# Optimization experiments

Hardware: AMD Instinct MI355X
Metric: run time of the kernel (lower is better)

## Reference

```python
import jax, jax.numpy as jnp
import numpy as np

ATT_RANGE = 10
R_FACTOR = 2
NHEAD = 8

def softsign(x):
    return x / (1.0 + jnp.abs(x))

def layer_norm(x, g, b, eps=1e-5):
    mu = jnp.mean(x, axis=-1, keepdims=True)
    var = jnp.var(x, axis=-1, keepdims=True)
    return (x - mu) / jnp.sqrt(var + eps) * g + b

def _forward(input_enc, input_dec, spkr_vec, speed, enc_w, enc_b, spkr_w, conv_w, speed_att_w,
             attproj_w, attproj_b, spd1_w, spd1_b, spd2_w, spd2_b, pre1_w, pre1_b, pre2_w, pre2_b,
             lstm_wih0, lstm_whh0, lstm_bih0, lstm_bhh0, lstm_wih1, lstm_whh1, lstm_bih1, lstm_bhh1,
             outl1_w, outl1_b, tr_inproj_w, tr_inproj_b, tr_out_w, tr_out_b, tr_ln1_g, tr_ln1_b,
             tr_ff1_w, tr_ff1_b, tr_ff2_w, tr_ff2_b, tr_ln2_g, tr_ln2_b, outl2_w, outl2_b, lengths_enc):
    N, T, ENC = input_enc.shape
    # first-step attention state: one-hot at t=0 (null_state branch)
    aw0 = jnp.zeros((N, T), input_enc.dtype).at[:, 0].set(1.0)
    # attention biases (null_bias branch)
    att_bias_enc = softsign(input_enc @ enc_w.T + enc_b)          # (N,T,ATT)
    att_bias_spkr = softsign(spkr_vec @ spkr_w.T)                  # (N,1,ATT)
    in_att_speed = (speed[:, None] @ speed_att_w.T)[:, None, :]    # (N,1,ATT)
    # location conv over previous attention: Conv1d(1, ATT, 31, pad 15, no bias)
    prev = jax.lax.conv_general_dilated(aw0[:, None, :], conv_w, (1,), [(15, 15)],
                                        dimension_numbers=('NCH', 'OIH', 'NCH'))  # (N,ATT,T)
    in_att_prev = prev.transpose(0, 2, 1)                          # (N,T,ATT)
    # hidden is None on first step -> in_att_dec = 0
    e = att_bias_enc + att_bias_spkr + in_att_prev + in_att_speed
    logit = jnp.tanh(e) @ attproj_w.T + attproj_b                  # (N,T,1)
    # windowed mask around argmax of previous attention (torch.no_grad)
    m = jnp.argmax(aw0, axis=1)                                    # (N,)
    t = jnp.arange(T)
    lm1 = lengths_enc - 1
    mask = ((t[None, :] >= (m - ATT_RANGE + 1)[:, None]) &
            (t[None, :] <= (m + ATT_RANGE - 1)[:, None]) &
            (t[None, :] <= lm1[:, None])).astype(logit.dtype)[..., None]
    w = jnp.exp(logit - jnp.max(logit, axis=1, keepdims=True)) * jax.lax.stop_gradient(mask)
    w = w / jnp.maximum(jnp.sum(jnp.abs(w), axis=1, keepdims=True), 1e-12)  # F.normalize p=1 dim=1
    # speed projection added to encoder features (eval mode: dropout off)
    sp = jnp.tanh(jax.nn.relu(speed[:, None] @ spd1_w.T + spd1_b) @ spd2_w.T + spd2_b)  # (N,ENC)
    enc2 = input_enc + sp[:, None, :]
    context = jnp.einsum('nt,ntc->nc', w[..., 0], enc2)[:, None, :]  # (N,1,ENC)
    # prenet on cat(input_dec, spkr)
    pin = jnp.concatenate([input_dec, spkr_vec[:, 0, :]], axis=-1)
    pre = jax.nn.relu(jax.nn.relu(pin @ pre1_w.T + pre1_b) @ pre2_w.T + pre2_b)[:, None, :]
    in_lstm = jnp.concatenate([pre, context, spkr_vec], axis=2)      # (N,1,DEC+ENC+SPK)
    # 2-layer LSTM, single timestep, zero initial state (h0=c0=0 -> Whh*h0 = 0)
    def lstm_step(x, wih, bih, bhh):
        g = x @ wih.T + bih + bhh
        i, f, gg, o = jnp.split(g, 4, axis=-1)
        c = jax.nn.sigmoid(i) * jnp.tanh(gg)
        return jax.nn.sigmoid(o) * jnp.tanh(c)
    h1 = lstm_step(in_lstm[:, 0, :], lstm_wih0, lstm_bih0, lstm_bhh0)
    h2 = lstm_step(h1, lstm_wih1, lstm_bih1, lstm_bhh1)
    out_lstm = h2[:, None, :]                                        # (N,1,4*DEC)
    # debug==14: cat(out_lstm, in_lstm) then seq-first for transformer
    x = jnp.concatenate([out_lstm, in_lstm], axis=2).transpose(1, 0, 2)  # (1,N,3136)
    x = x @ outl1_w.T + outl1_b                                      # (1,N,DEC)
    D = x.shape[-1]
    dh = D // NHEAD
    for l in range(tr_inproj_w.shape[0]):
        qkv = x @ tr_inproj_w[l].T + tr_inproj_b[l]
        q, k, v = jnp.split(qkv, 3, axis=-1)
        S, Nn, _ = q.shape
        qh = q.reshape(S, Nn, NHEAD, dh)
        kh = k.reshape(S, Nn, NHEAD, dh)
        vh = v.reshape(S, Nn, NHEAD, dh)
        a = jnp.einsum('snhd,tnhd->nhst', qh, kh) / jnp.sqrt(jnp.asarray(dh, x.dtype))
        a = jax.nn.softmax(a, axis=-1)
        att = jnp.einsum('nhst,tnhd->snhd', a, vh).reshape(S, Nn, D)
        att = att @ tr_out_w[l].T + tr_out_b[l]
        x = layer_norm(x + att, tr_ln1_g[l], tr_ln1_b[l])
        ff = jax.nn.relu(x @ tr_ff1_w[l].T + tr_ff1_b[l]) @ tr_ff2_w[l].T + tr_ff2_b[l]
        x = layer_norm(x + ff, tr_ln2_g[l], tr_ln2_b[l])
    out = (x @ outl2_w.T + outl2_b).transpose(1, 0, 2).reshape(N, R_FACTOR, -1)  # (N,2,80)
    return out, context

def setup_inputs():
    key = jax.random.key(0)
    ks = iter(jax.random.split(key, 64))
    def nrm(shape, s=0.05):
        return jax.random.normal(next(ks), shape, jnp.float32) * s
    N, T, ENC, ATT, DEC, OUT, SPK, L, FF = 32, 2048, 512, 256, 512, 80, 64, 2, 1024
    return dict(
        input_enc=nrm((N, T, ENC), 1.0),
        input_dec=nrm((N, OUT), 1.0),
        spkr_vec=nrm((N, 1, SPK), 1.0),
        speed=jax.random.uniform(next(ks), (N,), jnp.float32, 0.5, 1.5),
        lengths_enc=jnp.full((N,), T, dtype=jnp.int32),
        enc_w=nrm((ATT, ENC)), enc_b=nrm((ATT,)),
        spkr_w=nrm((ATT, SPK)),
        conv_w=nrm((ATT, 1, 31)),
        speed_att_w=nrm((ATT, 1)),
        attproj_w=nrm((1, ATT)), attproj_b=nrm((1,)),
        spd1_w=nrm((DEC, 1)), spd1_b=nrm((DEC,)), spd2_w=nrm((ENC, DEC)), spd2_b=nrm((ENC,)),
        pre1_w=nrm((2 * DEC, OUT + SPK)), pre1_b=nrm((2 * DEC,)),
        pre2_w=nrm((DEC, 2 * DEC)), pre2_b=nrm((DEC,)),
        lstm_wih0=nrm((16 * DEC, ENC + DEC + SPK)), lstm_whh0=nrm((16 * DEC, 4 * DEC)),
        lstm_bih0=nrm((16 * DEC,)), lstm_bhh0=nrm((16 * DEC,)),
        lstm_wih1=nrm((16 * DEC, 4 * DEC)), lstm_whh1=nrm((16 * DEC, 4 * DEC)),
        lstm_bih1=nrm((16 * DEC,)), lstm_bhh1=nrm((16 * DEC,)),
        outl1_w=nrm((DEC, ENC + DEC + SPK + 4 * DEC)), outl1_b=nrm((DEC,)),
        tr_inproj_w=nrm((L, 3 * DEC, DEC)), tr_inproj_b=nrm((L, 3 * DEC)),
        tr_out_w=nrm((L, DEC, DEC)), tr_out_b=nrm((L, DEC)),
        tr_ln1_g=jnp.ones((L, DEC)), tr_ln1_b=jnp.zeros((L, DEC)),
        tr_ff1_w=nrm((L, FF, DEC)), tr_ff1_b=nrm((L, FF)),
        tr_ff2_w=nrm((L, DEC, FF)), tr_ff2_b=nrm((L, DEC)),
        tr_ln2_g=jnp.ones((L, DEC)), tr_ln2_b=jnp.zeros((L, DEC)),
        outl2_w=nrm((R_FACTOR * OUT, DEC)), outl2_b=nrm((R_FACTOR * OUT,)),
    )

def reference(input_enc, input_dec, spkr_vec, speed, lengths_enc, enc_w, enc_b, spkr_w, conv_w,
              speed_att_w, attproj_w, attproj_b, spd1_w, spd1_b, spd2_w, spd2_b, pre1_w, pre1_b,
              pre2_w, pre2_b, lstm_wih0, lstm_whh0, lstm_bih0, lstm_bhh0, lstm_wih1, lstm_whh1,
              lstm_bih1, lstm_bhh1, outl1_w, outl1_b, tr_inproj_w, tr_inproj_b, tr_out_w, tr_out_b,
              tr_ln1_g, tr_ln1_b, tr_ff1_w, tr_ff1_b, tr_ff2_w, tr_ff2_b, tr_ln2_g, tr_ln2_b,
              outl2_w, outl2_b):
    return _forward(input_enc, input_dec, spkr_vec, speed, enc_w, enc_b, spkr_w, conv_w, speed_att_w,
                    attproj_w, attproj_b, spd1_w, spd1_b, spd2_w, spd2_b, pre1_w, pre1_b, pre2_w, pre2_b,
                    lstm_wih0, lstm_whh0, lstm_bih0, lstm_bhh0, lstm_wih1, lstm_whh1, lstm_bih1, lstm_bhh1,
                    outl1_w, outl1_b, tr_inproj_w, tr_inproj_b, tr_out_w, tr_out_b, tr_ln1_g, tr_ln1_b,
                    tr_ff1_w, tr_ff1_b, tr_ff2_w, tr_ff2_b, tr_ln2_g, tr_ln2_b, outl2_w, outl2_b, lengths_enc)
```

## Files before the change

### kernel.cpp

```cpp
#include <hip/hip_runtime.h>

typedef unsigned short u16;
typedef unsigned int u32;

__device__ __forceinline__ float bf2f(u16 u){ return __uint_as_float(((u32)u) << 16); }
__device__ __forceinline__ u16 f2bf(float f){
  u32 u = __float_as_uint(f);
  u32 r = u + 0x7fffu + ((u >> 16) & 1u);
  return (u16)(r >> 16);
}
__device__ __forceinline__ float lo2f(u32 u){ return __uint_as_float(u << 16); }
__device__ __forceinline__ float hi2f(u32 u){ return __uint_as_float(u & 0xffff0000u); }
__device__ __forceinline__ float uif(u32 u){ return __uint_as_float(u); }
__device__ __forceinline__ float sigf(float x){ return 1.0f / (1.0f + expf(-x)); }
__device__ __forceinline__ float wave_sum(float v){
  v += __shfl_xor(v, 1);  v += __shfl_xor(v, 2);  v += __shfl_xor(v, 4);
  v += __shfl_xor(v, 8);  v += __shfl_xor(v, 16); v += __shfl_xor(v, 32);
  return v;
}

template<int F32> __device__ __forceinline__ float IG(const void* p, size_t i){
  if constexpr (F32) return ((const float*)p)[i];
  else return bf2f(((const u16*)p)[i]);
}
template<int F32> __device__ __forceinline__ void OW(void* p, size_t i, float v){
  if constexpr (F32) ((float*)p)[i] = v;
  else ((u16*)p)[i] = f2bf(v);
}

__global__ void k_detect(const void* speed, int* flag)
{
  if (threadIdx.x == 0 && blockIdx.x == 0) {
    const u16* s = (const u16*)speed;
    int cnt = 0;
    #pragma unroll
    for (int i = 0; i < 8; ++i) {
      u16 v = s[2 * i];
      cnt += (v >= 0x3F00 && v <= 0x3FC0) ? 1 : 0;
    }
    flag[0] = (cnt >= 6) ? 0 : 1;
  }
}

template<int F32>
__global__ __launch_bounds__(256) void k_init(
    const int* __restrict__ flag,
    const void* __restrict__ dec, const void* __restrict__ spkr, const void* __restrict__ speed,
    const void* __restrict__ spd1_w, const void* __restrict__ spd1_b,
    float* __restrict__ pin, float* __restrict__ hspd, float* __restrict__ spkr_rn)
{
  if (flag[0] != F32) return;
  int idx = blockIdx.x * 256 + threadIdx.x;
  if (idx < 144 * 32) {
    int k = idx >> 5, n = idx & 31;
    float v = (k < 80) ? IG<F32>(dec, n * 80 + k) : IG<F32>(spkr, n * 64 + (k - 80));
    pin[idx] = v;
  } else if (idx < 144 * 32 + 512 * 32) {
    int j = idx - 144 * 32; int d = j >> 5, n = j & 31;
    float v = IG<F32>(speed, n) * IG<F32>(spd1_w, d) + IG<F32>(spd1_b, d);
    hspd[j] = fmaxf(v, 0.0f);
  } else if (idx < 144 * 32 + 512 * 32 + 64 * 32) {
    int j = idx - (144 * 32 + 512 * 32); int s = j >> 5, n = j & 31;
    spkr_rn[j] = IG<F32>(spkr, n * 64 + s);
  }
}

__device__ __forceinline__ float piece_fetch(int gk, int pn,
    const float* __restrict__ xa, int Ka, const float* __restrict__ xb, int Kb,
    const float* __restrict__ xc, int Kc, const float* __restrict__ xd)
{
  if (gk < Ka) return xa[(size_t)gk * 32 + pn];
  gk -= Ka;
  if (gk < Kb) return xb[(size_t)gk * 32 + pn];
  gk -= Kb;
  if (gk < Kc) return xc[(size_t)gk * 32 + pn];
  gk -= Kc;
  return xd[(size_t)gk * 32 + pn];
}

template<int F32>
__global__ __launch_bounds__(256) void k_gemv32(
    const int* __restrict__ flag,
    const float* __restrict__ xa, int Ka,
    const float* __restrict__ xb, int Kb,
    const float* __restrict__ xc, int Kc,
    const float* __restrict__ xd,
    const void* __restrict__ W,
    const void* __restrict__ bias1,
    const void* __restrict__ bias2,
    float* __restrict__ out,
    int K, int rowmap, int act)
{
  if (flag[0] != F32) return;
  __shared__ u32 xbuf[256][33];
  int tid = threadIdx.x;

  if constexpr (F32) {
    const int KCHE = 256;
    int n = tid & 31;
    int rl = tid >> 5;
    int r = blockIdx.x * 8 + rl;
    int wr = r;
    if (rowmap && r >= 2048) wr = r + 2048;
    float acc = 0.0f;
    for (int k0 = 0; k0 < K; k0 += KCHE) {
      int kc = K - k0; if (kc > KCHE) kc = KCHE;
      for (int p = tid; p < kc * 32; p += 256) {
        int pn = p & 31, kk = p >> 5;
        xbuf[kk][pn] = __float_as_uint(piece_fetch(k0 + kk, pn, xa, Ka, xb, Kb, xc, Kc, xd));
      }
      __syncthreads();
      const float4* wq = reinterpret_cast<const float4*>((const float*)W + (size_t)wr * (size_t)K + k0);
      for (int kk = 0; kk < kc; kk += 8) {
        float4 w0 = wq[(kk >> 2)];
        float4 w1 = wq[(kk >> 2) + 1];
        acc = fmaf(uif(xbuf[kk + 0][n]), w0.x, acc);
        acc = fmaf(uif(xbuf[kk + 1][n]), w0.y, acc);
        acc = fmaf(uif(xbuf[kk + 2][n]), w0.z, acc);
        acc = fmaf(uif(xbuf[kk + 3][n]), w0.w, acc);
        acc = fmaf(uif(xbuf[kk + 4][n]), w1.x, acc);
        acc = fmaf(uif(xbuf[kk + 5][n]), w1.y, acc);
        acc = fmaf(uif(xbuf[kk + 6][n]), w1.z, acc);
        acc = fmaf(uif(xbuf[kk + 7][n]), w1.w, acc);
      }
      __syncthreads();
    }
    if (bias1) acc += IG<F32>(bias1, wr);
    if (bias2) acc += IG<F32>(bias2, wr);
    if (act == 1) acc = fmaxf(acc, 0.0f);
    else if (act == 2) acc = tanhf(acc);
    out[(size_t)r * 32 + n] = acc;
  } else {
    int lane = tid & 63;
    int wv = tid >> 6;
    int r0 = blockIdx.x * 8 + wv * 2;
    int wr0 = (rowmap && r0 >= 2048) ? r0 + 2048 : r0;
    int wr1 = (rowmap && (r0 + 1) >= 2048) ? (r0 + 1) + 2048 : (r0 + 1);
    const u16* W16 = (const u16*)W;
    float acc0[32], acc1[32];
    #pragma unroll
    for (int i = 0; i < 32; ++i) { acc0[i] = 0.0f; acc1[i] = 0.0f; }

    for (int k0 = 0; k0 < K; k0 += 512) {
      int kc = K - k0; if (kc > 512) kc = 512;
      int pairs = kc >> 1;
      for (int p = tid; p < pairs * 32; p += 256) {
        int pn = p & 31, kk2 = p >> 5;
        int gk = k0 + 2 * kk2;
        float v0 = piece_fetch(gk,     pn, xa, Ka, xb, Kb, xc, Kc, xd);
        float v1 = piece_fetch(gk + 1, pn, xa, Ka, xb, Kb, xc, Kc, xd);
        xbuf[kk2][pn] = ((u32)f2bf(v1) << 16) | (u32)f2bf(v0);
      }
      __syncthreads();
      const u32* w0p = reinterpret_cast<const u32*>(W16 + (size_t)wr0 * (size_t)K + k0);
      const u32* w1p = reinterpret_cast<const u32*>(W16 + (size_t)wr1 * (size_t)K + k0);
      for (int p = lane; p < pairs; p += 64) {
        u32 wa = w0p[p];
        u32 wb = w1p[p];
        float wal = lo2f(wa), wah = hi2f(wa);
        float wbl = lo2f(wb), wbh = hi2f(wb);
        #pragma unroll
        for (int nn = 0; nn < 32; ++nn) {
          u32 xw = xbuf[p][nn];
          float xl = lo2f(xw), xh = hi2f(xw);
          acc0[nn] = fmaf(xl, wal, acc0[nn]);
          acc0[nn] = fmaf(xh, wah, acc0[nn]);
          acc1[nn] = fmaf(xl, wbl, acc1[nn]);
          acc1[nn] = fmaf(xh, wbh, acc1[nn]);
        }
      }
      __syncthreads();
    }

    float res = 0.0f;
    #pragma unroll
    for (int nn = 0; nn < 32; ++nn) {
      float s0 = wave_sum(acc0[nn]);
      float s1 = wave_sum(acc1[nn]);
      if (lane == nn)      res = s0;
      if (lane == 32 + nn) res = s1;
    }
    int r = r0 + (lane >> 5);
    int n_out = lane & 31;
    int wr = (rowmap && r >= 2048) ? r + 2048 : r;
    float acc = res;
    if (bias1) acc += IG<F32>(bias1, wr);
    if (bias2) acc += IG<F32>(bias2, wr);
    if (act == 1) acc = fmaxf(acc, 0.0f);
    else if (act == 2) acc = tanhf(acc);
    out[(size_t)r * 32 + n_out] = acc;
  }
}

template<int F32>
__global__ __launch_bounds__(256) void k_att_logit(
    const int* __restrict__ flag,
    const void* __restrict__ enc, const void* __restrict__ spkr, const void* __restrict__ speed,
    const void* __restrict__ enc_w, const void* __restrict__ enc_b, const void* __restrict__ spkr_w,
    const void* __restrict__ conv_w, const void* __restrict__ speed_att_w,
    const void* __restrict__ attproj_w, const void* __restrict__ attproj_b,
    float* __restrict__ logits)
{
  if (flag[0] != F32) return;
  int t = blockIdx.x;
  int n = blockIdx.y;
  int tid = threadIdx.x;
  __shared__ float encL[512];
  __shared__ float spkL[64];
  __shared__ float red[4];
  size_t ebase = ((size_t)n * 2048 + (size_t)t) * 512;
  encL[tid]       = IG<F32>(enc, ebase + tid);
  encL[tid + 256] = IG<F32>(enc, ebase + tid + 256);
  if (tid < 64) spkL[tid] = IG<F32>(spkr, n * 64 + tid);
  __syncthreads();

  int a = tid;
  float ss = 0.0f, d = 0.0f;
  if constexpr (F32) {
    const float4* sw = reinterpret_cast<const float4*>((const float*)spkr_w + (size_t)a * 64);
    #pragma unroll
    for (int i = 0; i < 16; ++i) {
      float4 wv = sw[i]; int c0 = i * 4;
      ss = fmaf(spkL[c0 + 0], wv.x, ss); ss = fmaf(spkL[c0 + 1], wv.y, ss);
      ss = fmaf(spkL[c0 + 2], wv.z, ss); ss = fmaf(spkL[c0 + 3], wv.w, ss);
    }
    const float4* ew = reinterpret_cast<const float4*>((const float*)enc_w + (size_t)a * 512);
    #pragma unroll 8
    for (int i = 0; i < 128; ++i) {
      float4 wv = ew[i]; int c0 = i * 4;
      d = fmaf(encL[c0 + 0], wv.x, d); d = fmaf(encL[c0 + 1], wv.y, d);
      d = fmaf(encL[c0 + 2], wv.z, d); d = fmaf(encL[c0 + 3], wv.w, d);
    }
  } else {
    const uint4* sw = reinterpret_cast<const uint4*>((const u16*)spkr_w + (size_t)a * 64);
    #pragma unroll
    for (int i = 0; i < 8; ++i) {
      uint4 wv = sw[i]; int c0 = i * 8;
      ss = fmaf(spkL[c0 + 0], lo2f(wv.x), ss); ss = fmaf(spkL[c0 + 1], hi2f(wv.x), ss);
      ss = fmaf(spkL[c0 + 2], lo2f(wv.y), ss); ss = fmaf(spkL[c0 + 3], hi2f(wv.y), ss);
      ss = fmaf(spkL[c0 + 4], lo2f(wv.z), ss); ss = fmaf(spkL[c0 + 5], hi2f(wv.z), ss);
      ss = fmaf(spkL[c0 + 6], lo2f(wv.w), ss); ss = fmaf(spkL[c0 + 7], hi2f(wv.w), ss);
    }
    const uint4* ew = reinterpret_cast<const uint4*>((const u16*)enc_w + (size_t)a * 512);
    #pragma unroll 8
    for (int i = 0; i < 64; ++i) {
      uint4 wv = ew[i]; int c0 = i * 8;
      d = fmaf(encL[c0 + 0], lo2f(wv.x), d); d = fmaf(encL[c0 + 1], hi2f(wv.x), d);
      d = fmaf(encL[c0 + 2], lo2f(wv.y), d); d = fmaf(encL[c0 + 3], hi2f(wv.y), d);
      d = fmaf(encL[c0 + 4], lo2f(wv.z), d); d = fmaf(encL[c0 + 5], hi2f(wv.z), d);
      d = fmaf(encL[c0 + 6], lo2f(wv.w), d); d = fmaf(encL[c0 + 7], hi2f(wv.w), d);
    }
  }
  float bspk = ss / (1.0f + fabsf(ss));
  float spd = IG<F32>(speed, n) * IG<F32>(speed_att_w, a);
  float arg = d + IG<F32>(enc_b, a);
  float be = arg / (1.0f + fabsf(arg));
  float e = be + bspk + IG<F32>(conv_w, a * 31 + (15 - t)) + spd;
  float p = tanhf(e) * IG<F32>(attproj_w, a);

  float s = wave_sum(p);
  int wid = tid >> 6;
  if ((tid & 63) == 0) red[wid] = s;
  __syncthreads();
  if (tid == 0) {
    logits[n * 16 + t] = red[0] + red[1] + red[2] + red[3] + IG<F32>(attproj_b, 0);
  }
}

template<int F32>
__global__ __launch_bounds__(256) void k_ctx2(
    const int* __restrict__ flag,
    const void* __restrict__ enc, const int* __restrict__ lengths,
    const float* __restrict__ logits, const float* __restrict__ sp,
    float* __restrict__ ctx, void* __restrict__ out)
{
  if (flag[0] != F32) return;
  int n = blockIdx.x, tid = threadIdx.x;
  __shared__ float wL[10];
  if (tid == 0) {
    int lm1 = lengths[n] - 1;
    float lf[10]; float m = -3.0e38f;
    #pragma unroll
    for (int t = 0; t < 10; ++t) { lf[t] = logits[n * 16 + t]; if (t <= lm1 && lf[t] > m) m = lf[t]; }
    float s = 0.0f, w[10];
    #pragma unroll
    for (int t = 0; t < 10; ++t) { w[t] = (t <= lm1) ? expf(lf[t] - m) : 0.0f; s += w[t]; }
    float dnm = fmaxf(s, 1e-12f);
    #pragma unroll
    for (int t = 0; t < 10; ++t) wL[t] = w[t] / dnm;
  }
  __syncthreads();
  for (int c = tid; c < 512; c += 256) {
    float spv = sp[(size_t)c * 32 + n];
    float acc = 0.0f;
    size_t base = (size_t)n * 2048 * 512 + c;
    #pragma unroll
    for (int t = 0; t < 10; ++t) acc += wL[t] * (IG<F32>(enc, base + (size_t)t * 512) + spv);
    ctx[(size_t)c * 32 + n] = acc;
    OW<F32>(out, 5120 + n * 512 + c, acc);
  }
}

__global__ __launch_bounds__(256) void k_act(const float* __restrict__ g, float* __restrict__ h)
{
  int f = blockIdx.x * 256 + threadIdx.x;
  int j = f >> 5, n = f & 31;
  float gi = g[(size_t)j * 32 + n];
  float gg = g[(size_t)(2048 + j) * 32 + n];
  float go = g[(size_t)(4096 + j) * 32 + n];
  float c = sigf(gi) * tanhf(gg);
  h[f] = sigf(go) * tanhf(c);
}

template<int F32>
__global__ __launch_bounds__(512) void k_attln(
    const int* __restrict__ flag,
    float* __restrict__ x,
    const void* __restrict__ Wv, const void* __restrict__ bv,
    const void* __restrict__ Wo, const void* __restrict__ bo,
    const void* __restrict__ lg, const void* __restrict__ lb)
{
  if (flag[0] != F32) return;
  int n = blockIdx.x, tid = threadIdx.x;
  __shared__ __align__(16) float xL[512];
  __shared__ __align__(16) float vL[512];
  __shared__ float red[18];
  xL[tid] = x[(size_t)tid * 32 + n];
  __syncthreads();

  const float4* x4 = reinterpret_cast<const float4*>(xL);
  float acc = 0.0f;
  if constexpr (F32) {
    const float4* wq = reinterpret_cast<const float4*>((const float*)Wv + (size_t)tid * 512);
    #pragma unroll 8
    for (int i = 0; i < 128; ++i) {
      float4 wv = wq[i]; float4 a0 = x4[i];
      acc = fmaf(a0.x, wv.x, acc); acc = fmaf(a0.y, wv.y, acc);
      acc = fmaf(a0.z, wv.z, acc); acc = fmaf(a0.w, wv.w, acc);
    }
  } else {
    const uint4* wq = reinterpret_cast<const uint4*>((const u16*)Wv + (size_t)tid * 512);
    #pragma unroll 8
    for (int i = 0; i < 64; ++i) {
      uint4 wv = wq[i];
      float4 a0 = x4[i * 2], a1 = x4[i * 2 + 1];
      acc = fmaf(a0.x, lo2f(wv.x), acc); acc = fmaf(a0.y, hi2f(wv.x), acc);
      acc = fmaf(a0.z, lo2f(wv.y), acc); acc = fmaf(a0.w, hi2f(wv.y), acc);
      acc = fmaf(a1.x, lo2f(wv.z), acc); acc = fmaf(a1.y, hi2f(wv.z), acc);
      acc = fmaf(a1.z, lo2f(wv.w), acc); acc = fmaf(a1.w, hi2f(wv.w), acc);
    }
  }
  vL[tid] = acc + IG<F32>(bv, tid);
  __syncthreads();

  const float4* v4 = reinterpret_cast<const float4*>(vL);
  float a2 = 0.0f;
  if constexpr (F32) {
    const float4* wq = reinterpret_cast<const float4*>((const float*)Wo + (size_t)tid * 512);
    #pragma unroll 8
    for (int i = 0; i < 128; ++i) {
      float4 wv = wq[i]; float4 a0 = v4[i];
      a2 = fmaf(a0.x, wv.x, a2); a2 = fmaf(a0.y, wv.y, a2);
      a2 = fmaf(a0.z, wv.z, a2); a2 = fmaf(a0.w, wv.w, a2);
    }
  } else {
    const uint4* wq = reinterpret_cast<const uint4*>((const u16*)Wo + (size_t)tid * 512);
    #pragma unroll 8
    for (int i = 0; i < 64; ++i) {
      uint4 wv = wq[i];
      float4 a0 = v4[i * 2], a1 = v4[i * 2 + 1];
      a2 = fmaf(a0.x, lo2f(wv.x), a2); a2 = fmaf(a0.y, hi2f(wv.x), a2);
      a2 = fmaf(a0.z, lo2f(wv.y), a2); a2 = fmaf(a0.w, hi2f(wv.y), a2);
      a2 = fmaf(a1.x, lo2f(wv.z), a2); a2 = fmaf(a1.y, hi2f(wv.z), a2);
      a2 = fmaf(a1.z, lo2f(wv.w), a2); a2 = fmaf(a1.w, hi2f(wv.w), a2);
    }
  }
  float y = xL[tid] + a2 + IG<F32>(bo, tid);

  float s1 = wave_sum(y), s2 = wave_sum(y * y);
  int wid = tid >> 6;
  if ((tid & 63) == 0) { red[wid] = s1; red[8 + wid] = s2; }
  __syncthreads();
  if (tid == 0) {
    float t1 = 0, t2 = 0;
    for (int i = 0; i < 8; ++i) { t1 += red[i]; t2 += red[8 + i]; }
    float mu = t1 * (1.0f / 512.0f);
    float var = t2 * (1.0f / 512.0f) - mu * mu;
    red[16] = mu; red[17] = rsqrtf(var + 1e-5f);
  }
  __syncthreads();
  float mu = red[16], rs = red[17];
  x[(size_t)tid * 32 + n] = (y - mu) * rs * IG<F32>(lg, tid) + IG<F32>(lb, tid);
}

template<int F32>
__global__ __launch_bounds__(512) void k_ff(
    const int* __restrict__ flag,
    float* __restrict__ x,
    const void* __restrict__ W1, const void* __restrict__ b1,
    const void* __restrict__ W2, const void* __restrict__ b2,
    const void* __restrict__ lg, const void* __restrict__ lb)
{
  if (flag[0] != F32) return;
  int n = blockIdx.x, tid = threadIdx.x;
  __shared__ __align__(16) float xL[512];
  __shared__ __align__(16) float hL[1024];
  __shared__ float red[18];
  xL[tid] = x[(size_t)tid * 32 + n];
  __syncthreads();

  const float4* x4 = reinterpret_cast<const float4*>(xL);
  for (int dd = tid; dd < 1024; dd += 512) {
    float acc = 0.0f;
    if constexpr (F32) {
      const float4* wq = reinterpret_cast<const float4*>((const float*)W1 + (size_t)dd * 512);
      #pragma unroll 8
      for (int i = 0; i < 128; ++i) {
        float4 wv = wq[i]; float4 a0 = x4[i];
        acc = fmaf(a0.x, wv.x, acc); acc = fmaf(a0.y, wv.y, acc);
        acc = fmaf(a0.z, wv.z, acc); acc = fmaf(a0.w, wv.w, acc);
      }
    } else {
      const uint4* wq = reinterpret_cast<const uint4*>((const u16*)W1 + (size_t)dd * 512);
      #pragma unroll 8
      for (int i = 0; i < 64; ++i) {
        uint4 wv = wq[i];
        float4 a0 = x4[i * 2], a1 = x4[i * 2 + 1];
        acc = fmaf(a0.x, lo2f(wv.x), acc); acc = fmaf(a0.y, hi2f(wv.x), acc);
        acc = fmaf(a0.z, lo2f(wv.y), acc); acc = fmaf(a0.w, hi2f(wv.y), acc);
        acc = fmaf(a1.x, lo2f(wv.z), acc); acc = fmaf(a1.y, hi2f(wv.z), acc);
        acc = fmaf(a1.z, lo2f(wv.w), acc); acc = fmaf(a1.w, hi2f(wv.w), acc);
      }
    }
    hL[dd] = fmaxf(acc + IG<F32>(b1, dd), 0.0f);
  }
  __syncthreads();

  const float4* h4 = reinterpret_cast<const float4*>(hL);
  float a2 = 0.0f;
  if constexpr (F32) {
    const float4* wq = reinterpret_cast<const float4*>((const float*)W2 + (size_t)tid * 1024);
    #pragma unroll 8
    for (int i = 0; i < 256; ++i) {
      float4 wv = wq[i]; float4 a0 = h4[i];
      a2 = fmaf(a0.x, wv.x, a2); a2 = fmaf(a0.y, wv.y, a2);
      a2 = fmaf(a0.z, wv.z, a2); a2 = fmaf(a0.w, wv.w, a2);
    }
  } else {
    const uint4* wq = reinterpret_cast<const uint4*>((const u16*)W2 + (size_t)tid * 1024);
    #pragma unroll 8
    for (int i = 0; i < 128; ++i) {
      uint4 wv = wq[i];
      float4 a0 = h4[i * 2], a1 = h4[i * 2 + 1];
      a2 = fmaf(a0.x, lo2f(wv.x), a2); a2 = fmaf(a0.y, hi2f(wv.x), a2);
      a2 = fmaf(a0.z, lo2f(wv.y), a2); a2 = fmaf(a0.w, hi2f(wv.y), a2);
      a2 = fmaf(a1.x, lo2f(wv.z), a2); a2 = fmaf(a1.y, hi2f(wv.z), a2);
      a2 = fmaf(a1.z, lo2f(wv.w), a2); a2 = fmaf(a1.w, hi2f(wv.w), a2);
    }
  }
  float y = xL[tid] + a2 + IG<F32>(b2, tid);

  float s1 = wave_sum(y), s2 = wave_sum(y * y);
  int wid = tid >> 6;
  if ((tid & 63) == 0) { red[wid] = s1; red[8 + wid] = s2; }
  __syncthreads();
  if (tid == 0) {
    float t1 = 0, t2 = 0;
    for (int i = 0; i < 8; ++i) { t1 += red[i]; t2 += red[8 + i]; }
    float mu = t1 * (1.0f / 512.0f);
    float var = t2 * (1.0f / 512.0f) - mu * mu;
    red[16] = mu; red[17] = rsqrtf(var + 1e-5f);
  }
  __syncthreads();
  float mu = red[16], rs = red[17];
  x[(size_t)tid * 32 + n] = (y - mu) * rs * IG<F32>(lg, tid) + IG<F32>(lb, tid);
}

template<int F32>
__global__ __launch_bounds__(256) void k_out2(
    const int* __restrict__ flag,
    const float* __restrict__ x, const void* __restrict__ W, const void* __restrict__ bias,
    void* __restrict__ out)
{
  if (flag[0] != F32) return;
  int n = blockIdx.x, tid = threadIdx.x;
  __shared__ __align__(16) float xL[512];
  xL[tid]       = x[(size_t)tid * 32 + n];
  xL[tid + 256] = x[(size_t)(tid + 256) * 32 + n];
  __syncthreads();
  if (tid < 160) {
    const float4* x4 = reinterpret_cast<const float4*>(xL);
    float acc = 0.0f;
    if constexpr (F32) {
      const float4* wq = reinterpret_cast<const float4*>((const float*)W + (size_t)tid * 512);
      #pragma unroll 8
      for (int i = 0; i < 128; ++i) {
        float4 wv = wq[i]; float4 a0 = x4[i];
        acc = fmaf(a0.x, wv.x, acc); acc = fmaf(a0.y, wv.y, acc);
        acc = fmaf(a0.z, wv.z, acc); acc = fmaf(a0.w, wv.w, acc);
      }
    } else {
      const uint4* wq = reinterpret_cast<const uint4*>((const u16*)W + (size_t)tid * 512);
      #pragma unroll 8
      for (int i = 0; i < 64; ++i) {
        uint4 wv = wq[i];
        float4 a0 = x4[i * 2], a1 = x4[i * 2 + 1];
        acc = fmaf(a0.x, lo2f(wv.x), acc); acc = fmaf(a0.y, hi2f(wv.x), acc);
        acc = fmaf(a0.z, lo2f(wv.y), acc); acc = fmaf(a0.w, hi2f(wv.y), acc);
        acc = fmaf(a1.x, lo2f(wv.z), acc); acc = fmaf(a1.y, hi2f(wv.z), acc);
        acc = fmaf(a1.z, lo2f(wv.w), acc); acc = fmaf(a1.w, hi2f(wv.w), acc);
      }
    }
    OW<F32>(out, n * 160 + tid, acc + IG<F32>(bias, tid));
  }
}

template<int F32>
static void run_pipeline(void* const* d_in, void* d_out, float* wsf, int* flag,
                         hipStream_t stream)
{
  const void* IN_ENC   = d_in[0];
  const void* IN_DEC   = d_in[1];
  const void* SPKR     = d_in[2];
  const void* SPEED    = d_in[3];
  const int*  LENGTHS  = (const int*)d_in[4];
  const void* ENC_W    = d_in[5];
  const void* ENC_B    = d_in[6];
  const void* SPKR_W   = d_in[7];
  const void* CONV_W   = d_in[8];
  const void* SPEEDA_W = d_in[9];
  const void* ATTP_W   = d_in[10];
  const void* ATTP_B   = d_in[11];
  const void* SPD1_W   = d_in[12];
  const void* SPD1_B   = d_in[13];
  const void* SPD2_W   = d_in[14];
  const void* SPD2_B   = d_in[15];
  const void* PRE1_W   = d_in[16];
  const void* PRE1_B   = d_in[17];
  const void* PRE2_W   = d_in[18];
  const void* PRE2_B   = d_in[19];
  const void* WIH0     = d_in[20];
  const void* BIH0     = d_in[22];
  const void* BHH0     = d_in[23];
  const void* WIH1     = d_in[24];
  const void* BIH1     = d_in[26];
  const void* BHH1     = d_in[27];
  const void* OUTL1_W  = d_in[28];
  const void* OUTL1_B  = d_in[29];
  const void* INPROJ_W = d_in[30];
  const void* INPROJ_B = d_in[31];
  const void* TOUT_W   = d_in[32];
  const void* TOUT_B   = d_in[33];
  const void* LN1_G    = d_in[34];
  const void* LN1_B    = d_in[35];
  const void* FF1_W    = d_in[36];
  const void* FF1_B    = d_in[37];
  const void* FF2_W    = d_in[38];
  const void* FF2_B    = d_in[39];
  const void* LN2_G    = d_in[40];
  const void* LN2_B    = d_in[41];
  const void* OUTL2_W  = d_in[42];
  const void* OUTL2_B  = d_in[43];

  float* pin     = wsf + 0;
  float* hspd    = wsf + 4608;
  float* spkr_rn = wsf + 20992;
  float* sp      = wsf + 23040;
  float* logits  = wsf + 39424;
  float* ctx     = wsf + 39936;
  float* prehid  = wsf + 56320;
  float* pre     = wsf + 89088;
  float* g0      = wsf + 105472;
  float* h1      = wsf + 302080;
  float* g1      = g0;
  float* h2      = wsf + 367616;
  float* xs      = wsf + 433152;

  k_init<F32><<<90, 256, 0, stream>>>(flag, IN_DEC, SPKR, SPEED, SPD1_W, SPD1_B,
                                      pin, hspd, spkr_rn);
  k_gemv32<F32><<<64, 256, 0, stream>>>(flag, hspd, 512, hspd, 0, hspd, 0, hspd,
                                        SPD2_W, SPD2_B, nullptr, sp, 512, 0, 2);
  k_att_logit<F32><<<dim3(10, 32), 256, 0, stream>>>(flag, IN_ENC, SPKR, SPEED,
                                        ENC_W, ENC_B, SPKR_W, CONV_W, SPEEDA_W,
                                        ATTP_W, ATTP_B, logits);
  k_ctx2<F32><<<32, 256, 0, stream>>>(flag, IN_ENC, LENGTHS, logits, sp, ctx, d_out);
  k_gemv32<F32><<<128, 256, 0, stream>>>(flag, pin, 144, pin, 0, pin, 0, pin,
                                         PRE1_W, PRE1_B, nullptr, prehid, 144, 0, 1);
  k_gemv32<F32><<<64, 256, 0, stream>>>(flag, prehid, 1024, prehid, 0, prehid, 0, prehid,
                                        PRE2_W, PRE2_B, nullptr, pre, 1024, 0, 1);
  k_gemv32<F32><<<768, 256, 0, stream>>>(flag, pre, 512, ctx, 512, spkr_rn, 64, pre,
                                         WIH0, BIH0, BHH0, g0, 1088, 1, 0);
  k_act<<<256, 256, 0, stream>>>(g0, h1);
  k_gemv32<F32><<<768, 256, 0, stream>>>(flag, h1, 2048, h1, 0, h1, 0, h1,
                                         WIH1, BIH1, BHH1, g1, 2048, 1, 0);
  k_act<<<256, 256, 0, stream>>>(g1, h2);
  k_gemv32<F32><<<64, 256, 0, stream>>>(flag, h2, 2048, pre, 512, ctx, 512, spkr_rn,
                                        OUTL1_W, OUTL1_B, nullptr, xs, 3136, 0, 0);

  for (int l = 0; l < 2; ++l) {
    size_t e = F32 ? 1 : 1;
    const char* Wv = (const char*)INPROJ_W; const char* bv = (const char*)INPROJ_B;
    const char* Wo = (const char*)TOUT_W;   const char* bo = (const char*)TOUT_B;
    const char* W1 = (const char*)FF1_W;    const char* W2 = (const char*)FF2_W;
    int esz = F32 ? 4 : 2;
    k_attln<F32><<<32, 512, 0, stream>>>(flag, xs,
        Wv + ((size_t)l * 786432 + 524288) * esz,
        bv + ((size_t)l * 1536 + 1024) * esz,
        Wo + ((size_t)l * 262144) * esz,
        bo + ((size_t)l * 512) * esz,
        (const char*)LN1_G + (size_t)l * 512 * esz,
        (const char*)LN1_B + (size_t)l * 512 * esz);
    k_ff<F32><<<32, 512, 0, stream>>>(flag, xs,
        W1 + ((size_t)l * 524288) * esz,
        (const char*)FF1_B + (size_t)l * 1024 * esz,
        W2 + ((size_t)l * 524288) * esz,
        (const char*)FF2_B + (size_t)l * 512 * esz,
        (const char*)LN2_G + (size_t)l * 512 * esz,
        (const char*)LN2_B + (size_t)l * 512 * esz);
    (void)e;
  }

  k_out2<F32><<<32, 256, 0, stream>>>(flag, xs, OUTL2_W, OUTL2_B, d_out);
}

extern "C" void kernel_launch(void* const* d_in, const int* in_sizes, int n_in,
                              void* d_out, int out_size, void* d_ws, size_t ws_size,
                              hipStream_t stream)
{
  float* wsf = (float*)d_ws;
  int* flag = (int*)(wsf + 458752);

  k_detect<<<1, 64, 0, stream>>>(d_in[3], flag);

  run_pipeline<0>(d_in, d_out, wsf, flag, stream);
  run_pipeline<1>(d_in, d_out, wsf, flag, stream);
}
```

Measured before the change: 772.2 us.

## Replace per-sample transformer kernels with batched gemv32 calls plus separate layernorm

The fused attention and feed-forward kernels processed one batch column per block, so every block reread the full weight matrices, 32 times in total. These are replaced with the shared k_gemv32 kernel, which reads each weight row once for all 32 batch columns, followed by a small residual-plus-layernorm kernel. The gemv32 K-chunk is also halved (128 for fp32, 256 for bf16) to shrink shared memory and allow more resident blocks. In exchange there are more kernel launches and intermediate buffers written to global workspace, and those buffers reuse the g0 region.

Result: faster. 723.3 us (-6.3%).

```diff
diff --git a/kernel.cpp b/kernel.cpp
--- a/kernel.cpp
+++ b/kernel.cpp
@@ -92,11 +92,11 @@
     int K, int rowmap, int act)
 {
   if (flag[0] != F32) return;
-  __shared__ u32 xbuf[256][33];
+  __shared__ u32 xbuf[128][33];
+  const int KCHE = F32 ? 128 : 256;
   int tid = threadIdx.x;
 
   if constexpr (F32) {
-    const int KCHE = 256;
     int n = tid & 31;
     int rl = tid >> 5;
     int r = blockIdx.x * 8 + rl;
@@ -141,8 +141,8 @@
     #pragma unroll
     for (int i = 0; i < 32; ++i) { acc0[i] = 0.0f; acc1[i] = 0.0f; }
 
-    for (int k0 = 0; k0 < K; k0 += 512) {
-      int kc = K - k0; if (kc > 512) kc = 512;
+    for (int k0 = 0; k0 < K; k0 += KCHE) {
+      int kc = K - k0; if (kc > KCHE) kc = KCHE;
       int pairs = kc >> 1;
       for (int p = tid; p < pairs * 32; p += 256) {
         int pn = p & 31, kk2 = p >> 5;
@@ -313,153 +313,15 @@
 }
 
 template<int F32>
-__global__ __launch_bounds__(512) void k_attln(
+__global__ __launch_bounds__(512) void k_ln(
     const int* __restrict__ flag,
-    float* __restrict__ x,
-    const void* __restrict__ Wv, const void* __restrict__ bv,
-    const void* __restrict__ Wo, const void* __restrict__ bo,
+    float* __restrict__ x, const float* __restrict__ delta,
     const void* __restrict__ lg, const void* __restrict__ lb)
 {
   if (flag[0] != F32) return;
   int n = blockIdx.x, tid = threadIdx.x;
-  __shared__ __align__(16) float xL[512];
-  __shared__ __align__(16) float vL[512];
   __shared__ float red[18];
-  xL[tid] = x[(size_t)tid * 32 + n];
-  __syncthreads();
-
-  const float4* x4 = reinterpret_cast<const float4*>(xL);
-  float acc = 0.0f;
-  if constexpr (F32) {
-    const float4* wq = reinterpret_cast<const float4*>((const float*)Wv + (size_t)tid * 512);
-    #pragma unroll 8
-    for (int i = 0; i < 128; ++i) {
-      float4 wv = wq[i]; float4 a0 = x4[i];
-      acc = fmaf(a0.x, wv.x, acc); acc = fmaf(a0.y, wv.y, acc);
-      acc = fmaf(a0.z, wv.z, acc); acc = fmaf(a0.w, wv.w, acc);
-    }
-  } else {
-    const uint4* wq = reinterpret_cast<const uint4*>((const u16*)Wv + (size_t)tid * 512);
-    #pragma unroll 8
-    for (int i = 0; i < 64; ++i) {
-      uint4 wv = wq[i];
-      float4 a0 = x4[i * 2], a1 = x4[i * 2 + 1];
-      acc = fmaf(a0.x, lo2f(wv.x), acc); acc = fmaf(a0.y, hi2f(wv.x), acc);
-      acc = fmaf(a0.z, lo2f(wv.y), acc); acc = fmaf(a0.w, hi2f(wv.y), acc);
-      acc = fmaf(a1.x, lo2f(wv.z), acc); acc = fmaf(a1.y, hi2f(wv.z), acc);
-      acc = fmaf(a1.z, lo2f(wv.w), acc); acc = fmaf(a1.w, hi2f(wv.w), acc);
-    }
-  }
-  vL[tid] = acc + IG<F32>(bv, tid);
-  __syncthreads();
-
-  const float4* v4 = reinterpret_cast<const float4*>(vL);
-  float a2 = 0.0f;
-  if constexpr (F32) {
-    const float4* wq = reinterpret_cast<const float4*>((const float*)Wo + (size_t)tid * 512);
-    #pragma unroll 8
-    for (int i = 0; i < 128; ++i) {
-      float4 wv = wq[i]; float4 a0 = v4[i];
-      a2 = fmaf(a0.x, wv.x, a2); a2 = fmaf(a0.y, wv.y, a2);
-      a2 = fmaf(a0.z, wv.z, a2); a2 = fmaf(a0.w, wv.w, a2);
-    }
-  } else {
-    const uint4* wq = reinterpret_cast<const uint4*>((const u16*)Wo + (size_t)tid * 512);
-    #pragma unroll 8
-    for (int i = 0; i < 64; ++i) {
-      uint4 wv = wq[i];
-      float4 a0 = v4[i * 2], a1 = v4[i * 2 + 1];
-      a2 = fmaf(a0.x, lo2f(wv.x), a2); a2 = fmaf(a0.y, hi2f(wv.x), a2);
-      a2 = fmaf(a0.z, lo2f(wv.y), a2); a2 = fmaf(a0.w, hi2f(wv.y), a2);
-      a2 = fmaf(a1.x, lo2f(wv.z), a2); a2 = fmaf(a1.y, hi2f(wv.z), a2);
-      a2 = fmaf(a1.z, lo2f(wv.w), a2); a2 = fmaf(a1.w, hi2f(wv.w), a2);
-    }
-  }
-  float y = xL[tid] + a2 + IG<F32>(bo, tid);
-
-  float s1 = wave_sum(y), s2 = wave_sum(y * y);
-  int wid = tid >> 6;
-  if ((tid & 63) == 0) { red[wid] = s1; red[8 + wid] = s2; }
-  __syncthreads();
-  if (tid == 0) {
-    float t1 = 0, t2 = 0;
-    for (int i = 0; i < 8; ++i) { t1 += red[i]; t2 += red[8 + i]; }
-    float mu = t1 * (1.0f / 512.0f);
-    float var = t2 * (1.0f / 512.0f) - mu * mu;
-    red[16] = mu; red[17] = rsqrtf(var + 1e-5f);
-  }
-  __syncthreads();
-  float mu = red[16], rs = red[17];
-  x[(size_t)tid * 32 + n] = (y - mu) * rs * IG<F32>(lg, tid) + IG<F32>(lb, tid);
-}
-
-template<int F32>
-__global__ __launch_bounds__(512) void k_ff(
-    const int* __restrict__ flag,
-    float* __restrict__ x,
-    const void* __restrict__ W1, const void* __restrict__ b1,
-    const void* __restrict__ W2, const void* __restrict__ b2,
-    const void* __restrict__ lg, const void* __restrict__ lb)
-{
-  if (flag[0] != F32) return;
-  int n = blockIdx.x, tid = threadIdx.x;
-  __shared__ __align__(16) float xL[512];
-  __shared__ __align__(16) float hL[1024];
-  __shared__ float red[18];
-  xL[tid] = x[(size_t)tid * 32 + n];
-  __syncthreads();
-
-  const float4* x4 = reinterpret_cast<const float4*>(xL);
-  for (int dd = tid; dd < 1024; dd += 512) {
-    float acc = 0.0f;
-    if constexpr (F32) {
-      const float4* wq = reinterpret_cast<const float4*>((const float*)W1 + (size_t)dd * 512);
-      #pragma unroll 8
-      for (int i = 0; i < 128; ++i) {
-        float4 wv = wq[i]; float4 a0 = x4[i];
-        acc = fmaf(a0.x, wv.x, acc); acc = fmaf(a0.y, wv.y, acc);
-        acc = fmaf(a0.z, wv.z, acc); acc = fmaf(a0.w, wv.w, acc);
-      }
-    } else {
-      const uint4* wq = reinterpret_cast<const uint4*>((const u16*)W1 + (size_t)dd * 512);
-      #pragma unroll 8
-      for (int i = 0; i < 64; ++i) {
-        uint4 wv = wq[i];
-        float4 a0 = x4[i * 2], a1 = x4[i * 2 + 1];
-        acc = fmaf(a0.x, lo2f(wv.x), acc); acc = fmaf(a0.y, hi2f(wv.x), acc);
-        acc = fmaf(a0.z, lo2f(wv.y), acc); acc = fmaf(a0.w, hi2f(wv.y), acc);
-        acc = fmaf(a1.x, lo2f(wv.z), acc); acc = fmaf(a1.y, hi2f(wv.z), acc);
-        acc = fmaf(a1.z, lo2f(wv.w), acc); acc = fmaf(a1.w, hi2f(wv.w), acc);
-      }
-    }
-    hL[dd] = fmaxf(acc + IG<F32>(b1, dd), 0.0f);
-  }
-  __syncthreads();
-
-  const float4* h4 = reinterpret_cast<const float4*>(hL);
-  float a2 = 0.0f;
-  if constexpr (F32) {
-    const float4* wq = reinterpret_cast<const float4*>((const float*)W2 + (size_t)tid * 1024);
-    #pragma unroll 8
-    for (int i = 0; i < 256; ++i) {
-      float4 wv = wq[i]; float4 a0 = h4[i];
-      a2 = fmaf(a0.x, wv.x, a2); a2 = fmaf(a0.y, wv.y, a2);
-      a2 = fmaf(a0.z, wv.z, a2); a2 = fmaf(a0.w, wv.w, a2);
-    }
-  } else {
-    const uint4* wq = reinterpret_cast<const uint4*>((const u16*)W2 + (size_t)tid * 1024);
-    #pragma unroll 8
-    for (int i = 0; i < 128; ++i) {
-      uint4 wv = wq[i];
-      float4 a0 = h4[i * 2], a1 = h4[i * 2 + 1];
-      a2 = fmaf(a0.x, lo2f(wv.x), a2); a2 = fmaf(a0.y, hi2f(wv.x), a2);
-      a2 = fmaf(a0.z, lo2f(wv.y), a2); a2 = fmaf(a0.w, hi2f(wv.y), a2);
-      a2 = fmaf(a1.x, lo2f(wv.z), a2); a2 = fmaf(a1.y, hi2f(wv.z), a2);
-      a2 = fmaf(a1.z, lo2f(wv.w), a2); a2 = fmaf(a1.w, hi2f(wv.w), a2);
-    }
-  }
-  float y = xL[tid] + a2 + IG<F32>(b2, tid);
-
+  float y = x[(size_t)tid * 32 + n] + delta[(size_t)tid * 32 + n];
   float s1 = wave_sum(y), s2 = wave_sum(y * y);
   int wid = tid >> 6;
   if ((tid & 63) == 0) { red[wid] = s1; red[8 + wid] = s2; }
@@ -575,6 +437,10 @@
   float* g1      = g0;
   float* h2      = wsf + 367616;
   float* xs      = wsf + 433152;
+  float* vbuf    = wsf + 105472;
+  float* abuf    = wsf + 121856;
+  float* hbuf    = wsf + 138240;
+  float* fbuf    = wsf + 171008;
 
   k_init<F32><<<90, 256, 0, stream>>>(flag, IN_DEC, SPKR, SPEED, SPD1_W, SPD1_B,
                                       pin, hspd, spkr_rn);
@@ -598,26 +464,28 @@
                                         OUTL1_W, OUTL1_B, nullptr, xs, 3136, 0, 0);
 
   for (int l = 0; l < 2; ++l) {
-    size_t e = F32 ? 1 : 1;
     const char* Wv = (const char*)INPROJ_W; const char* bv = (const char*)INPROJ_B;
     const char* Wo = (const char*)TOUT_W;   const char* bo = (const char*)TOUT_B;
     const char* W1 = (const char*)FF1_W;    const char* W2 = (const char*)FF2_W;
     int esz = F32 ? 4 : 2;
-    k_attln<F32><<<32, 512, 0, stream>>>(flag, xs,
+    k_gemv32<F32><<<64, 256, 0, stream>>>(flag, xs, 512, xs, 0, xs, 0, xs,
         Wv + ((size_t)l * 786432 + 524288) * esz,
-        bv + ((size_t)l * 1536 + 1024) * esz,
+        bv + ((size_t)l * 1536 + 1024) * esz, nullptr, vbuf, 512, 0, 0);
+    k_gemv32<F32><<<64, 256, 0, stream>>>(flag, vbuf, 512, vbuf, 0, vbuf, 0, vbuf,
         Wo + ((size_t)l * 262144) * esz,
-        bo + ((size_t)l * 512) * esz,
+        bo + ((size_t)l * 512) * esz, nullptr, abuf, 512, 0, 0);
+    k_ln<F32><<<32, 512, 0, stream>>>(flag, xs, abuf,
         (const char*)LN1_G + (size_t)l * 512 * esz,
         (const char*)LN1_B + (size_t)l * 512 * esz);
-    k_ff<F32><<<32, 512, 0, stream>>>(flag, xs,
+    k_gemv32<F32><<<128, 256, 0, stream>>>(flag, xs, 512, xs, 0, xs, 0, xs,
         W1 + ((size_t)l * 524288) * esz,
-        (const char*)FF1_B + (size_t)l * 1024 * esz,
+        (const char*)FF1_B + (size_t)l * 1024 * esz, nullptr, hbuf, 512, 0, 1);
+    k_gemv32<F32><<<64, 256, 0, stream>>>(flag, hbuf, 1024, hbuf, 0, hbuf, 0, hbuf,
         W2 + ((size_t)l * 524288) * esz,
-        (const char*)FF2_B + (size_t)l * 512 * esz,
+        (const char*)FF2_B + (size_t)l * 512 * esz, nullptr, fbuf, 1024, 0, 0);
+    k_ln<F32><<<32, 512, 0, stream>>>(flag, xs, fbuf,
         (const char*)LN2_G + (size_t)l * 512 * esz,
         (const char*)LN2_B + (size_t)l * 512 * esz);
-    (void)e;
   }
 
   k_out2<F32><<<32, 256, 0, stream>>>(flag, xs, OUTL2_W, OUTL2_B, d_out);
```
